# Kernel tuning notes

Hardware: AMD Instinct MI355X
Metric: run time of the kernel (lower is better)

The kernel has to match this reference:

```python
import jax, jax.numpy as jnp
import numpy as np

H, C = 4, 32            # heads, per-head channels (hidden_dim)
F_IN = 128
N_NODES = 50000
N_EDGES = 800000
N_GRAPHS = 64
EPS_SM = 1e-16          # PyG softmax denom eps
EPS_BN = 1e-5


def gat_layer(x, W, a_src, a_dst, b, src, dst, n):
    # x: [N, Fin]; W: [Fin, H*C]; a_src/a_dst: [H, C]; b: [H*C]
    h = (x @ W).reshape(n, H, C)                      # [N,H,C]
    e_src = jnp.einsum('nhc,hc->nh', h, a_src)        # [N,H]
    e_dst = jnp.einsum('nhc,hc->nh', h, a_dst)
    e = jax.nn.leaky_relu(e_src[src] + e_dst[dst], 0.2)  # [E,H]
    m = jax.lax.stop_gradient(jax.ops.segment_max(e, dst, num_segments=n))
    ex = jnp.exp(e - m[dst])
    denom = jax.ops.segment_sum(ex, dst, num_segments=n)
    alpha = ex / (denom[dst] + EPS_SM)                # softmax per destination node
    out = jax.ops.segment_sum(h[src] * alpha[..., None], dst, num_segments=n)
    return out.reshape(n, H * C) + b


def batchnorm(x, gamma, beta):
    # training-mode BN over the node dimension (biased variance)
    mu = x.mean(0)
    var = x.var(0)
    return (x - mu) * jax.lax.rsqrt(var + EPS_BN) * gamma + beta


def setup_inputs() -> dict:
    key = jax.random.key(0)
    ks = jax.random.split(key, 24)
    D = H * C  # 128

    def lin(k, fan_in, shape):
        return jax.random.normal(k, shape, jnp.float32) / np.sqrt(fan_in)

    inp = {
        'x': jax.random.normal(ks[0], (N_NODES, F_IN), jnp.float32),
        'edge_index': jax.random.randint(ks[1], (2, N_EDGES), 0, N_NODES, jnp.int64),
        'node_types': jax.random.randint(ks[2], (N_NODES,), 0, 2, jnp.int64),
        'batch': jnp.sort(jax.random.randint(ks[3], (N_NODES,), 0, N_GRAPHS, jnp.int64)),
        # GAT layer 1 (F_IN -> H*C)
        'W1': lin(ks[4], F_IN, (F_IN, D)), 'as1': lin(ks[5], C, (H, C)),
        'ad1': lin(ks[6], C, (H, C)), 'b1': jnp.zeros((D,), jnp.float32),
        'g1': jnp.ones((D,), jnp.float32), 'be1': jnp.zeros((D,), jnp.float32),
        # GAT layer 2 (D -> D)
        'W2': lin(ks[7], D, (D, D)), 'as2': lin(ks[8], C, (H, C)),
        'ad2': lin(ks[9], C, (H, C)), 'b2': jnp.zeros((D,), jnp.float32),
        'g2': jnp.ones((D,), jnp.float32), 'be2': jnp.zeros((D,), jnp.float32),
        # GAT layer 3 (D -> D)
        'W3': lin(ks[10], D, (D, D)), 'as3': lin(ks[11], C, (H, C)),
        'ad3': lin(ks[12], C, (H, C)), 'b3': jnp.zeros((D,), jnp.float32),
        'g3': jnp.ones((D,), jnp.float32), 'be3': jnp.zeros((D,), jnp.float32),
        # MLP head
        'fc1_w': lin(ks[13], D, (D, C)), 'fc1_b': jnp.zeros((C,), jnp.float32),
        'fc2_w': lin(ks[14], C, (C, 1)), 'fc2_b': jnp.zeros((1,), jnp.float32),
    }
    return inp


def reference(x, edge_index, node_types, batch,
              W1, as1, ad1, b1, g1, be1,
              W2, as2, ad2, b2, g2, be2,
              W3, as3, ad3, b3, g3, be3,
              fc1_w, fc1_b, fc2_w, fc2_b):
    n = x.shape[0]
    # PyG GATConv adds self-loops by default
    loops = jnp.arange(n, dtype=edge_index.dtype)
    src = jnp.concatenate([edge_index[0], loops])
    dst = jnp.concatenate([edge_index[1], loops])
    aw = jnp.where(node_types == 0, 1.5, 1.0).astype(x.dtype)[:, None]  # [N,1]

    h = gat_layer(x, W1, as1, ad1, b1, src, dst, n) * aw
    h = jax.nn.relu(batchnorm(h, g1, be1))
    h = gat_layer(h, W2, as2, ad2, b2, src, dst, n) * aw
    h = jax.nn.relu(batchnorm(h, g2, be2))
    h = gat_layer(h, W3, as3, ad3, b3, src, dst, n) * aw
    h = jax.nn.relu(batchnorm(h, g3, be3))

    # global mean pool over graphs
    sums = jax.ops.segment_sum(h, batch, num_segments=N_GRAPHS)
    cnt = jax.ops.segment_sum(jnp.ones((n,), h.dtype), batch, num_segments=N_GRAPHS)
    pooled = sums / jnp.maximum(cnt, 1.0)[:, None]     # [G, H*C]

    out = jax.nn.relu(pooled @ fc1_w + fc1_b) @ fc2_w + fc2_b  # [G, 1]
    return out
```

## Files before the change

kernel.cpp:

```cpp
#include <hip/hip_runtime.h>
#include <hip/hip_bf16.h>
#include <math.h>

#define NN 50000
#define EE 800000
#define ET_ 850000
#define NG 64
#define NB 196
#define PB 1024
#define GB 391
#define NBK 196
#define BCAP 5120
#define GATB 2048

typedef __attribute__((ext_vector_type(8))) short bf16x8;
typedef __attribute__((ext_vector_type(4))) float f32x4;
typedef __attribute__((ext_vector_type(4))) _Float16 h16x4;

__device__ __forceinline__ void bsplit(float v, ushort& h, ushort& l){
  unsigned u = __float_as_uint(v);
  unsigned hb = (u + 0x7fffu + ((u >> 16) & 1u)) >> 16;
  h = (ushort)hb;
  float hf = __uint_as_float(hb << 16);
  float r = v - hf;
  unsigned ur = __float_as_uint(r);
  l = (ushort)((ur + 0x7fffu + ((ur >> 16) & 1u)) >> 16);
}

__global__ __launch_bounds__(256) void convw(const float* __restrict__ W,
    ushort* __restrict__ wfrag){
  int idx = blockIdx.x*256 + threadIdx.x;
  if (idx >= 128*128) return;
  int c = idx & 127, k = idx >> 7;
  float v = W[idx];
  ushort h, lo;
  bsplit(v, h, lo);
  int dest = (((c>>4)*4 + (k>>5))*64 + (((k&31)>>3)<<4 | (c&15)))*8 + (k&7);
  wfrag[dest] = h;
  wfrag[16384 + dest] = lo;
}

__global__ __launch_bounds__(256) void convea(const float* __restrict__ W,
    const float* __restrict__ as_, const float* __restrict__ ad_,
    ushort* __restrict__ eafrag){
  const int t = threadIdx.x;
  const int kb = t >> 6, l = t & 63;
  const int col = l & 15, krow = (l >> 4) * 8;
  #pragma unroll
  for (int j = 0; j < 8; j++){
    int k = kb*32 + krow + j;
    float v = 0.f;
    if (col < 8){
      int h = col & 3;
      const float* a  = (col < 4) ? (as_ + h*32) : (ad_ + h*32);
      const float* wr = W + (size_t)k*128 + h*32;
      float acc = 0.f;
      #pragma unroll
      for (int c = 0; c < 32; c++) acc += wr[c]*a[c];
      v = acc;
    }
    ushort hi, lo;
    bsplit(v, hi, lo);
    eafrag[(kb*64 + l)*8 + j] = hi;
    eafrag[2048 + (kb*64 + l)*8 + j] = lo;
  }
}

__global__ __launch_bounds__(512) void gemm_fused(const float* __restrict__ X,
    const ushort* __restrict__ wfrag, const ushort* __restrict__ eafrag,
    const float* __restrict__ scale, const float* __restrict__ shift,
    _Float16* __restrict__ H, float* __restrict__ esrc, float* __restrict__ edst, int N){
  __shared__ ushort wl[32768];
  const int tid = threadIdx.x;
  #pragma unroll
  for (int i = 0; i < 8; i++){
    int e = (i*512 + tid) * 8;
    *(bf16x8*)(wl + e) = *(const bf16x8*)(wfrag + e);
  }
  const int w  = tid >> 6;
  const int l  = tid & 63;
  const int lr = l & 15;
  const int lg = l >> 4;
  const int lk = lg * 8;
  const int arow = blockIdx.x*128 + w*16 + lr;
  const bool avl = (arow < N);
  const size_t abase = (size_t)(avl ? arow : 0) * 128;
  bf16x8 ahi[4], alo[4];
  #pragma unroll
  for (int kb = 0; kb < 4; kb++){
    float a[8];
    if (avl){
      *(float4*)(a)   = *(const float4*)(X + abase + kb*32 + lk);
      *(float4*)(a+4) = *(const float4*)(X + abase + kb*32 + lk + 4);
    } else {
      #pragma unroll
      for (int j=0;j<8;j++) a[j] = 0.f;
    }
    if (scale){
      float s[8], b[8];
      *(float4*)(s)   = *(const float4*)(scale + kb*32 + lk);
      *(float4*)(s+4) = *(const float4*)(scale + kb*32 + lk + 4);
      *(float4*)(b)   = *(const float4*)(shift + kb*32 + lk);
      *(float4*)(b+4) = *(const float4*)(shift + kb*32 + lk + 4);
      #pragma unroll
      for (int j=0;j<8;j++) a[j] = fmaxf(fmaf(a[j], s[j], b[j]), 0.f);
    }
    #pragma unroll
    for (int j=0;j<8;j++){
      ushort hh2, ll2;
      bsplit(a[j], hh2, ll2);
      ahi[kb][j] = (short)hh2;
      alo[kb][j] = (short)ll2;
    }
  }
  __syncthreads();
  const int crowb = blockIdx.x*128 + w*16 + lg*4;
  #pragma unroll
  for (int ct = 0; ct < 8; ct++){
    f32x4 acc = {0.f,0.f,0.f,0.f};
    #pragma unroll
    for (int kb = 0; kb < 4; kb++){
      const int fi = ((ct*4 + kb)*64 + l) * 8;
      bf16x8 bhf = *(const bf16x8*)(wl + fi);
      bf16x8 blf = *(const bf16x8*)(wl + 16384 + fi);
      acc = __builtin_amdgcn_mfma_f32_16x16x32_bf16(ahi[kb], bhf, acc, 0, 0, 0);
      acc = __builtin_amdgcn_mfma_f32_16x16x32_bf16(ahi[kb], blf, acc, 0, 0, 0);
      acc = __builtin_amdgcn_mfma_f32_16x16x32_bf16(alo[kb], bhf, acc, 0, 0, 0);
    }
    #pragma unroll
    for (int j = 0; j < 4; j++){
      int r = crowb + j;
      if (r < N) H[(size_t)r*128 + ct*16 + lr] = (_Float16)acc[j];
    }
  }
  {
    f32x4 acc = {0.f,0.f,0.f,0.f};
    #pragma unroll
    for (int kb = 0; kb < 4; kb++){
      bf16x8 bhf = *(const bf16x8*)(eafrag + (kb*64 + l)*8);
      bf16x8 blf = *(const bf16x8*)(eafrag + 2048 + (kb*64 + l)*8);
      acc = __builtin_amdgcn_mfma_f32_16x16x32_bf16(ahi[kb], bhf, acc, 0, 0, 0);
      acc = __builtin_amdgcn_mfma_f32_16x16x32_bf16(ahi[kb], blf, acc, 0, 0, 0);
      acc = __builtin_amdgcn_mfma_f32_16x16x32_bf16(alo[kb], bhf, acc, 0, 0, 0);
    }
    if (lr < 8){
      #pragma unroll
      for (int j = 0; j < 4; j++){
        int r = crowb + j;
        if (r < N){
          if (lr < 4) esrc[r*4 + lr] = acc[j];
          else        edst[r*4 + lr - 4] = acc[j];
        }
      }
    }
  }
}

__global__ __launch_bounds__(256) void bin_scatter(const int* __restrict__ ei,
    int* __restrict__ btail, int2* __restrict__ bkt){
  __shared__ int cnt[NBK];
  __shared__ int base[NBK];
  const int t = threadIdx.x;
  for (int i = t; i < NBK; i += 256) cnt[i] = 0;
  __syncthreads();
  int sv[8], dv[8], bv[8], lr[8];
  const int e0 = blockIdx.x*2048;
  #pragma unroll
  for (int k = 0; k < 8; k++){
    int i = e0 + k*256 + t;
    sv[k] = -1;
    if (i < ET_){
      int s, d;
      if (i < EE){ s = ei[i]; d = ei[EE + i]; } else { s = i - EE; d = s; }
      sv[k] = s; dv[k] = d; bv[k] = d >> 8;
      lr[k] = atomicAdd(&cnt[bv[k]], 1);
    }
  }
  __syncthreads();
  for (int i = t; i < NBK; i += 256){
    int c = cnt[i];
    base[i] = c ? atomicAdd(&btail[i], c) : 0;
  }
  __syncthreads();
  #pragma unroll
  for (int k = 0; k < 8; k++){
    if (sv[k] >= 0){
      int p = base[bv[k]] + lr[k];
      if (p < BCAP) bkt[bv[k]*BCAP + p] = make_int2(sv[k], dv[k]);
    }
  }
}

__global__ __launch_bounds__(256) void bucket_count(const int* __restrict__ btail,
    const int2* __restrict__ bkt, int* __restrict__ cnt){
  __shared__ int c256[256];
  const int b = blockIdx.x, t = threadIdx.x;
  c256[t] = 0; __syncthreads();
  int n = btail[b]; if (n > BCAP) n = BCAP;
  for (int i = t; i < n; i += 256){
    int d = bkt[b*BCAP + i].y;
    atomicAdd(&c256[d & 255], 1);
  }
  __syncthreads();
  int node = b*256 + t;
  if (node < NN) cnt[node] = c256[t];
}

__global__ __launch_bounds__(256) void scan_partial(const int* __restrict__ cnt,
    int* __restrict__ rowptr, int* __restrict__ bsum){
  __shared__ int sh[256];
  const int t = threadIdx.x;
  const int i = blockIdx.x*256 + t;
  int v = (i < NN) ? cnt[i] : 0;
  sh[t] = v; __syncthreads();
  for (int o=1;o<256;o<<=1){
    int u = (t>=o) ? sh[t-o] : 0;
    __syncthreads();
    sh[t] += u;
    __syncthreads();
  }
  if (i < NN) rowptr[i] = sh[t] - v;
  if (t == 255) bsum[blockIdx.x] = sh[255];
}

__global__ __launch_bounds__(256) void scan_bsum(int* __restrict__ bsum){
  __shared__ int sh[256];
  const int t = threadIdx.x;
  int v = (t < NB) ? bsum[t] : 0;
  sh[t] = v; __syncthreads();
  for (int o=1;o<256;o<<=1){
    int u = (t>=o) ? sh[t-o] : 0;
    __syncthreads();
    sh[t] += u;
    __syncthreads();
  }
  if (t < NB) bsum[t] = sh[t] - v;
}

__global__ __launch_bounds__(256) void scan_add(int* __restrict__ rowptr,
    const int* __restrict__ bsum){
  const int i = blockIdx.x*256 + threadIdx.x;
  if (i < NN) rowptr[i] += bsum[blockIdx.x];
  if (i == NN) rowptr[NN] = ET_;
}

__global__ __launch_bounds__(256) void bucket_scatter(const int* __restrict__ btail,
    const int2* __restrict__ bkt, const int* __restrict__ rowptr,
    int* __restrict__ csr_src){
  __shared__ int h256[256];
  const int b = blockIdx.x, t = threadIdx.x;
  int node = b*256 + t;
  h256[t] = (node < NN) ? rowptr[node] : 0;
  __syncthreads();
  int n = btail[b]; if (n > BCAP) n = BCAP;
  for (int i = t; i < n; i += 256){
    int2 e = bkt[b*BCAP + i];
    int pos = atomicAdd(&h256[e.y & 255], 1);
    csr_src[pos] = e.x;
  }
}

__global__ __launch_bounds__(256) void gat_fused(const int* __restrict__ rowptr,
    const int* __restrict__ csr_src, const float* __restrict__ esrc,
    const float* __restrict__ edst, const _Float16* __restrict__ hbuf,
    const float* __restrict__ bias, const int* __restrict__ ntype,
    float* __restrict__ y, float* __restrict__ bnpart){
  __shared__ int2 pk[4][64][4];
  const int w    = threadIdx.x >> 6;
  const int lane = threadIdx.x & 63;
  const int c4   = (lane & 31) * 4;
  const int eh   = lane >> 5;
  const int head = (lane & 31) >> 3;
  const int2* pp = &pk[w][eh][head];

  float bs0=0.f,bs1=0.f,bs2=0.f,bs3=0.f,bq0=0.f,bq1=0.f,bq2=0.f,bq3=0.f;
  const float4 bb = *(const float4*)(bias + c4);

  for (int d = blockIdx.x*4 + w; d < NN; d += GATB*4){
    const int beg = rowptr[d], end = rowptr[d+1];
    const float4 ed4 = *(const float4*)(edst + (size_t)d*4);
    float dn0=0.f, dn1=0.f, dn2=0.f, dn3=0.f;
    float4 acc0 = make_float4(0.f,0.f,0.f,0.f);
    float4 acc1 = make_float4(0.f,0.f,0.f,0.f);

    for (int j0 = beg; j0 < end; j0 += 64){
      int j = j0 + lane;
      int s = d;
      float ex0=0.f, ex1=0.f, ex2=0.f, ex3=0.f;
      if (j < end){
        s = csr_src[j];
        float4 es = *(const float4*)(esrc + (size_t)s*4);
        float e0 = es.x + ed4.x; e0 = (e0 > 0.f) ? e0 : 0.2f*e0;
        float e1 = es.y + ed4.y; e1 = (e1 > 0.f) ? e1 : 0.2f*e1;
        float e2 = es.z + ed4.z; e2 = (e2 > 0.f) ? e2 : 0.2f*e2;
        float e3 = es.w + ed4.w; e3 = (e3 > 0.f) ? e3 : 0.2f*e3;
        ex0 = expf(e0); ex1 = expf(e1); ex2 = expf(e2); ex3 = expf(e3);
        dn0 += ex0; dn1 += ex1; dn2 += ex2; dn3 += ex3;
      }
      int4 w0 = make_int4(s, __float_as_int(ex0), s, __float_as_int(ex1));
      int4 w1 = make_int4(s, __float_as_int(ex2), s, __float_as_int(ex3));
      *(int4*)&pk[w][lane][0] = w0;
      *(int4*)&pk[w][lane][2] = w1;
      int cnt2 = end - j0; if (cnt2 > 64) cnt2 = 64;
      const int npair = (cnt2 + 1) >> 1;
      int p = 0;
      #pragma unroll 2
      for (; p + 2 <= npair; p += 2){
        int2 va = pp[p*8];
        int2 vb = pp[p*8 + 8];
        float wa = __int_as_float(va.y);
        float wb = __int_as_float(vb.y);
        h16x4 ha = *(const h16x4*)(hbuf + (size_t)va.x*128 + c4);
        h16x4 hb = *(const h16x4*)(hbuf + (size_t)vb.x*128 + c4);
        acc0.x = fmaf((float)ha.x, wa, acc0.x);
        acc0.y = fmaf((float)ha.y, wa, acc0.y);
        acc0.z = fmaf((float)ha.z, wa, acc0.z);
        acc0.w = fmaf((float)ha.w, wa, acc0.w);
        acc1.x = fmaf((float)hb.x, wb, acc1.x);
        acc1.y = fmaf((float)hb.y, wb, acc1.y);
        acc1.z = fmaf((float)hb.z, wb, acc1.z);
        acc1.w = fmaf((float)hb.w, wb, acc1.w);
      }
      if (p < npair){
        int2 va = pp[p*8];
        float wa = __int_as_float(va.y);
        h16x4 ha = *(const h16x4*)(hbuf + (size_t)va.x*128 + c4);
        acc0.x = fmaf((float)ha.x, wa, acc0.x);
        acc0.y = fmaf((float)ha.y, wa, acc0.y);
        acc0.z = fmaf((float)ha.z, wa, acc0.z);
        acc0.w = fmaf((float)ha.w, wa, acc0.w);
      }
    }
    #pragma unroll
    for (int o = 32; o; o >>= 1){
      dn0 += __shfl_xor(dn0, o);
      dn1 += __shfl_xor(dn1, o);
      dn2 += __shfl_xor(dn2, o);
      dn3 += __shfl_xor(dn3, o);
    }
    float dsel = (head==0) ? dn0 : (head==1) ? dn1 : (head==2) ? dn2 : dn3;
    float inv = 1.f / (dsel + 1e-16f);
    float4 acc;
    acc.x = acc0.x + acc1.x;
    acc.y = acc0.y + acc1.y;
    acc.z = acc0.z + acc1.z;
    acc.w = acc0.w + acc1.w;
    acc.x += __shfl_xor(acc.x, 32);
    acc.y += __shfl_xor(acc.y, 32);
    acc.z += __shfl_xor(acc.z, 32);
    acc.w += __shfl_xor(acc.w, 32);
    if (eh == 0){
      float aw = (ntype[d] == 0) ? 1.5f : 1.0f;
      float4 o4;
      o4.x = (acc.x*inv + bb.x) * aw;
      o4.y = (acc.y*inv + bb.y) * aw;
      o4.z = (acc.z*inv + bb.z) * aw;
      o4.w = (acc.w*inv + bb.w) * aw;
      *(float4*)(y + (size_t)d*128 + c4) = o4;
      bs0 += o4.x; bs1 += o4.y; bs2 += o4.z; bs3 += o4.w;
      bq0 += o4.x*o4.x; bq1 += o4.y*o4.y; bq2 += o4.z*o4.z; bq3 += o4.w*o4.w;
    }
  }
  __syncthreads();
  float* bnp = (float*)pk;
  if (eh == 0){
    float* q = bnp + (w*32 + (lane & 31))*8;
    q[0]=bs0; q[1]=bs1; q[2]=bs2; q[3]=bs3;
    q[4]=bq0; q[5]=bq1; q[6]=bq2; q[7]=bq3;
  }
  __syncthreads();
  const int t = threadIdx.x;
  const int c = t & 127, stat = t >> 7;
  float v = 0.f;
  #pragma unroll
  for (int ww = 0; ww < 4; ww++)
    v += bnp[(ww*32 + (c>>2))*8 + stat*4 + (c&3)];
  bnpart[(size_t)blockIdx.x*256 + t] = v;
}

__global__ __launch_bounds__(256) void bn_reduce(const float* __restrict__ bnpart,
    double* __restrict__ bnsum, double* __restrict__ bnsumsq){
  const int t = threadIdx.x, b = blockIdx.x;
  float acc = 0.f;
  #pragma unroll 4
  for (int j = 0; j < GATB/64; j++)
    acc += bnpart[(size_t)(b*(GATB/64) + j)*256 + t];
  const int c = t & 127;
  if (t < 128) atomicAdd(bnsum + c, (double)acc);
  else         atomicAdd(bnsumsq + c, (double)acc);
}

__global__ void bn_final(const double* __restrict__ bnsum, const double* __restrict__ bnsumsq,
    const float* __restrict__ gma, const float* __restrict__ bta,
    float* __restrict__ scale, float* __restrict__ shift, int N){
  int c = threadIdx.x;
  double mu  = bnsum[c] / N;
  double var = bnsumsq[c] / N - mu*mu;
  if (var < 0.0) var = 0.0;
  float inv = (float)(1.0 / sqrt(var + 1e-5));
  float sc  = inv * gma[c];
  scale[c] = sc;
  shift[c] = bta[c] - (float)mu * sc;
}

__global__ __launch_bounds__(256) void pool_partial(const float* __restrict__ y,
    const int* __restrict__ batch, const float* __restrict__ scale,
    const float* __restrict__ shift, float* __restrict__ pooled){
  const int t = threadIdx.x;
  const int c = t & 127;
  const int sub = t >> 7;
  const int per = (NN + PB - 1) / PB;
  const int n0 = blockIdx.x * per;
  int n1 = n0 + per; if (n1 > NN) n1 = NN;
  const float sc = scale[c], sh = shift[c];
  float acc = 0.f;
  int curg = -1;
  for (int n = n0 + sub; n < n1; n += 2){
    int g = batch[n];
    if (g != curg){
      if (curg >= 0) unsafeAtomicAdd(pooled + (size_t)curg*128 + c, acc);
      curg = g; acc = 0.f;
    }
    float v = y[(size_t)n*128 + c];
    acc += fmaxf(fmaf(v, sc, sh), 0.f);
  }
  if (curg >= 0) unsafeAtomicAdd(pooled + (size_t)curg*128 + c, acc);
}

__global__ __launch_bounds__(128) void mlp_head(const float* __restrict__ pooled,
    const int* __restrict__ batch, const float* __restrict__ fc1w,
    const float* __restrict__ fc1b, const float* __restrict__ fc2w,
    const float* __restrict__ fc2b, float* __restrict__ out){
  __shared__ float psh[128];
  __shared__ float hid[32];
  const int g = blockIdx.x, t = threadIdx.x;
  int lo = 0, hi = NN;
  while (lo < hi){ int mid = (lo+hi)>>1; if (batch[mid] < g) lo = mid+1; else hi = mid; }
  const int beg = lo;
  lo = beg; hi = NN;
  while (lo < hi){ int mid = (lo+hi)>>1; if (batch[mid] < g+1) lo = mid+1; else hi = mid; }
  int cntn = lo - beg; if (cntn < 1) cntn = 1;
  psh[t] = pooled[(size_t)g*128 + t] / (float)cntn;
  __syncthreads();
  if (t < 32){
    float a = fc1b[t];
    for (int k=0;k<128;k++) a += psh[k]*fc1w[k*32+t];
    a = (a > 0.f) ? a : 0.f;
    hid[t] = a * fc2w[t];
  }
  __syncthreads();
  if (t == 0){
    float sacc = fc2b[0];
    #pragma unroll
    for (int j=0;j<32;j++) sacc += hid[j];
    out[g] = sacc;
  }
}

extern "C" void kernel_launch(void* const* d_in, const int* in_sizes, int n_in,
                              void* d_out, int out_size, void* d_ws, size_t ws_size,
                              hipStream_t stream){
  const float* x     = (const float*)d_in[0];
  const int*   ei    = (const int*)d_in[1];
  const int*   ntype = (const int*)d_in[2];
  const int*   batch = (const int*)d_in[3];
  const float* Wl[3]  = {(const float*)d_in[4],  (const float*)d_in[10], (const float*)d_in[16]};
  const float* asl[3] = {(const float*)d_in[5],  (const float*)d_in[11], (const float*)d_in[17]};
  const float* adl[3] = {(const float*)d_in[6],  (const float*)d_in[12], (const float*)d_in[18]};
  const float* bl[3]  = {(const float*)d_in[7],  (const float*)d_in[13], (const float*)d_in[19]};
  const float* gl[3]  = {(const float*)d_in[8],  (const float*)d_in[14], (const float*)d_in[20]};
  const float* bel[3] = {(const float*)d_in[9],  (const float*)d_in[15], (const float*)d_in[21]};
  const float* fc1w = (const float*)d_in[22];
  const float* fc1b = (const float*)d_in[23];
  const float* fc2w = (const float*)d_in[24];
  const float* fc2b = (const float*)d_in[25];

  char* base = (char*)d_ws;
  size_t off = 0;
  auto alloc = [&](size_t bytes)->char*{
    size_t o = (off + 255) & ~(size_t)255; off = o + bytes; return base + o;
  };
  _Float16* hbuf = (_Float16*)alloc((size_t)NN*128*2);
  float* y       = (float*)alloc((size_t)NN*128*4);
  ushort* wfrag  = (ushort*)alloc((size_t)32768*2);
  ushort* eafrag = (ushort*)alloc((size_t)4096*2);
  float* esrc    = (float*)alloc((size_t)NN*4*4);
  float* edst    = (float*)alloc((size_t)NN*4*4);
  int*   cnt     = (int*)  alloc((size_t)NN*4);
  int*   rowptr  = (int*)  alloc((size_t)(NN+1)*4);
  int*   csr_src = (int*)  alloc((size_t)ET_*4);
  int*   btail   = (int*)  alloc((size_t)NBK*4);
  int2*  bkt     = (int2*) alloc((size_t)NBK*BCAP*8);
  int*   bsum    = (int*)  alloc((size_t)NB*4);
  float* bnpart  = (float*)alloc((size_t)GATB*256*4);
  double* bnsum  = (double*)alloc(128*8);
  double* bnsumsq= (double*)alloc(128*8);
  float* scale   = (float*)alloc(128*4);
  float* shift   = (float*)alloc(128*4);
  float* pooled  = (float*)alloc((size_t)NG*128*4);
  if (off > ws_size) return;

  hipMemsetAsync(btail, 0, (size_t)NBK*4, stream);
  hipMemsetAsync(pooled, 0, (size_t)NG*128*4, stream);
  bin_scatter<<<(ET_+2047)/2048, 256, 0, stream>>>(ei, btail, bkt);
  bucket_count<<<NBK, 256, 0, stream>>>(btail, bkt, cnt);
  scan_partial<<<NB, 256, 0, stream>>>(cnt, rowptr, bsum);
  scan_bsum<<<1, 256, 0, stream>>>(bsum);
  scan_add<<<NB, 256, 0, stream>>>(rowptr, bsum);
  bucket_scatter<<<NBK, 256, 0, stream>>>(btail, bkt, rowptr, csr_src);

  for (int l = 0; l < 3; l++){
    const float* in = (l==0) ? x : y;
    const float* scl = (l==0) ? nullptr : scale;
    const float* shf = (l==0) ? nullptr : shift;
    hipMemsetAsync(bnsum, 0, 128*8*2, stream);
    convw<<<64, 256, 0, stream>>>(Wl[l], wfrag);
    convea<<<1, 256, 0, stream>>>(Wl[l], asl[l], adl[l], eafrag);
    gemm_fused<<<GB, 512, 0, stream>>>(in, wfrag, eafrag, scl, shf,
                                       hbuf, esrc, edst, NN);
    gat_fused<<<GATB, 256, 0, stream>>>(rowptr, csr_src, esrc, edst, hbuf,
                                        bl[l], ntype, y, bnpart);
    bn_reduce<<<64, 256, 0, stream>>>(bnpart, bnsum, bnsumsq);
    bn_final<<<1, 128, 0, stream>>>(bnsum, bnsumsq, gl[l], bel[l], scale, shift, NN);
  }
  pool_partial<<<PB, 256, 0, stream>>>(y, batch, scale, shift, pooled);
  mlp_head<<<NG, 128, 0, stream>>>(pooled, batch, fc1w, fc1b, fc2w, fc2b, (float*)d_out);
}
```

Measured before the change: 435.2 us.

## Widen GAT gather to 8 channels per lane, 4 edges per wave; merge weight-prep kernels

The aggregation kernel now has each lane gather 8 fp16 channels (16-byte loads), so a wave processes 4 edges at once instead of 2. Partial sums are reduced across lanes with two xor-shuffle steps. The BN partial-sum layout is adjusted to match the new lane mapping. The grid grows from 2048 to 6144 blocks, and the two small weight-conversion kernels are merged into one launch to save a kernel launch per layer. With 6144 blocks, bn_reduce's 64 blocks now read 96 partials each.

Result: no change. 432.3 us (-0.7%).

```diff
diff --git a/kernel.cpp b/kernel.cpp
--- a/kernel.cpp
+++ b/kernel.cpp
@@ -11,11 +11,11 @@
 #define GB 391
 #define NBK 196
 #define BCAP 5120
-#define GATB 2048
+#define GATB 6144
 
 typedef __attribute__((ext_vector_type(8))) short bf16x8;
 typedef __attribute__((ext_vector_type(4))) float f32x4;
-typedef __attribute__((ext_vector_type(4))) _Float16 h16x4;
+typedef __attribute__((ext_vector_type(8))) _Float16 h16x8;
 
 __device__ __forceinline__ void bsplit(float v, ushort& h, ushort& l){
   unsigned u = __float_as_uint(v);
@@ -27,42 +27,40 @@
   l = (ushort)((ur + 0x7fffu + ((ur >> 16) & 1u)) >> 16);
 }
 
-__global__ __launch_bounds__(256) void convw(const float* __restrict__ W,
-    ushort* __restrict__ wfrag){
-  int idx = blockIdx.x*256 + threadIdx.x;
-  if (idx >= 128*128) return;
-  int c = idx & 127, k = idx >> 7;
-  float v = W[idx];
-  ushort h, lo;
-  bsplit(v, h, lo);
-  int dest = (((c>>4)*4 + (k>>5))*64 + (((k&31)>>3)<<4 | (c&15)))*8 + (k&7);
-  wfrag[dest] = h;
-  wfrag[16384 + dest] = lo;
-}
-
-__global__ __launch_bounds__(256) void convea(const float* __restrict__ W,
+__global__ __launch_bounds__(256) void convwa(const float* __restrict__ W,
     const float* __restrict__ as_, const float* __restrict__ ad_,
-    ushort* __restrict__ eafrag){
+    ushort* __restrict__ wfrag, ushort* __restrict__ eafrag){
   const int t = threadIdx.x;
-  const int kb = t >> 6, l = t & 63;
-  const int col = l & 15, krow = (l >> 4) * 8;
-  #pragma unroll
-  for (int j = 0; j < 8; j++){
-    int k = kb*32 + krow + j;
-    float v = 0.f;
-    if (col < 8){
-      int h = col & 3;
-      const float* a  = (col < 4) ? (as_ + h*32) : (ad_ + h*32);
-      const float* wr = W + (size_t)k*128 + h*32;
-      float acc = 0.f;
-      #pragma unroll
-      for (int c = 0; c < 32; c++) acc += wr[c]*a[c];
-      v = acc;
-    }
-    ushort hi, lo;
-    bsplit(v, hi, lo);
-    eafrag[(kb*64 + l)*8 + j] = hi;
-    eafrag[2048 + (kb*64 + l)*8 + j] = lo;
+  if (blockIdx.x < 64){
+    int idx = blockIdx.x*256 + t;
+    int c = idx & 127, k = idx >> 7;
+    float v = W[idx];
+    ushort h, lo;
+    bsplit(v, h, lo);
+    int dest = (((c>>4)*4 + (k>>5))*64 + (((k&31)>>3)<<4 | (c&15)))*8 + (k&7);
+    wfrag[dest] = h;
+    wfrag[16384 + dest] = lo;
+  } else {
+    const int kb = t >> 6, l = t & 63;
+    const int col = l & 15, krow = (l >> 4) * 8;
+    #pragma unroll
+    for (int j = 0; j < 8; j++){
+      int k = kb*32 + krow + j;
+      float v = 0.f;
+      if (col < 8){
+        int h = col & 3;
+        const float* a  = (col < 4) ? (as_ + h*32) : (ad_ + h*32);
+        const float* wr = W + (size_t)k*128 + h*32;
+        float acc = 0.f;
+        #pragma unroll
+        for (int c = 0; c < 32; c++) acc += wr[c]*a[c];
+        v = acc;
+      }
+      ushort hi, lo;
+      bsplit(v, hi, lo);
+      eafrag[(kb*64 + l)*8 + j] = hi;
+      eafrag[2048 + (kb*64 + l)*8 + j] = lo;
+    }
   }
 }
 
@@ -268,20 +266,24 @@
   __shared__ int2 pk[4][64][4];
   const int w    = threadIdx.x >> 6;
   const int lane = threadIdx.x & 63;
-  const int c4   = (lane & 31) * 4;
-  const int eh   = lane >> 5;
-  const int head = (lane & 31) >> 3;
-  const int2* pp = &pk[w][eh][head];
-
-  float bs0=0.f,bs1=0.f,bs2=0.f,bs3=0.f,bq0=0.f,bq1=0.f,bq2=0.f,bq3=0.f;
-  const float4 bb = *(const float4*)(bias + c4);
+  const int e    = lane >> 4;
+  const int c8   = lane & 15;
+  const int hd   = c8 >> 2;
+  const int2* pg = &pk[w][e][hd];
+
+  float bs[8], bq[8];
+  #pragma unroll
+  for (int k=0;k<8;k++){ bs[k]=0.f; bq[k]=0.f; }
+  const float4 bbA = *(const float4*)(bias + c8*8);
+  const float4 bbB = *(const float4*)(bias + c8*8 + 4);
 
   for (int d = blockIdx.x*4 + w; d < NN; d += GATB*4){
     const int beg = rowptr[d], end = rowptr[d+1];
     const float4 ed4 = *(const float4*)(edst + (size_t)d*4);
     float dn0=0.f, dn1=0.f, dn2=0.f, dn3=0.f;
-    float4 acc0 = make_float4(0.f,0.f,0.f,0.f);
-    float4 acc1 = make_float4(0.f,0.f,0.f,0.f);
+    float acc[8];
+    #pragma unroll
+    for (int k=0;k<8;k++) acc[k]=0.f;
 
     for (int j0 = beg; j0 < end; j0 += 64){
       int j = j0 + lane;
@@ -302,33 +304,14 @@
       *(int4*)&pk[w][lane][0] = w0;
       *(int4*)&pk[w][lane][2] = w1;
       int cnt2 = end - j0; if (cnt2 > 64) cnt2 = 64;
-      const int npair = (cnt2 + 1) >> 1;
-      int p = 0;
+      const int ngrp = (cnt2 + 3) >> 2;
       #pragma unroll 2
-      for (; p + 2 <= npair; p += 2){
-        int2 va = pp[p*8];
-        int2 vb = pp[p*8 + 8];
-        float wa = __int_as_float(va.y);
-        float wb = __int_as_float(vb.y);
-        h16x4 ha = *(const h16x4*)(hbuf + (size_t)va.x*128 + c4);
-        h16x4 hb = *(const h16x4*)(hbuf + (size_t)vb.x*128 + c4);
-        acc0.x = fmaf((float)ha.x, wa, acc0.x);
-        acc0.y = fmaf((float)ha.y, wa, acc0.y);
-        acc0.z = fmaf((float)ha.z, wa, acc0.z);
-        acc0.w = fmaf((float)ha.w, wa, acc0.w);
-        acc1.x = fmaf((float)hb.x, wb, acc1.x);
-        acc1.y = fmaf((float)hb.y, wb, acc1.y);
-        acc1.z = fmaf((float)hb.z, wb, acc1.z);
-        acc1.w = fmaf((float)hb.w, wb, acc1.w);
-      }
-      if (p < npair){
-        int2 va = pp[p*8];
-        float wa = __int_as_float(va.y);
-        h16x4 ha = *(const h16x4*)(hbuf + (size_t)va.x*128 + c4);
-        acc0.x = fmaf((float)ha.x, wa, acc0.x);
-        acc0.y = fmaf((float)ha.y, wa, acc0.y);
-        acc0.z = fmaf((float)ha.z, wa, acc0.z);
-        acc0.w = fmaf((float)ha.w, wa, acc0.w);
+      for (int g = 0; g < ngrp; g++){
+        int2 v = pg[g*16];
+        float wg = __int_as_float(v.y);
+        h16x8 hv = *(const h16x8*)(hbuf + (size_t)v.x*128 + c8*8);
+        #pragma unroll
+        for (int k=0;k<8;k++) acc[k] = fmaf((float)hv[k], wg, acc[k]);
       }
     }
     #pragma unroll
@@ -338,35 +321,36 @@
       dn2 += __shfl_xor(dn2, o);
       dn3 += __shfl_xor(dn3, o);
     }
-    float dsel = (head==0) ? dn0 : (head==1) ? dn1 : (head==2) ? dn2 : dn3;
+    float dsel = (hd==0) ? dn0 : (hd==1) ? dn1 : (hd==2) ? dn2 : dn3;
     float inv = 1.f / (dsel + 1e-16f);
-    float4 acc;
-    acc.x = acc0.x + acc1.x;
-    acc.y = acc0.y + acc1.y;
-    acc.z = acc0.z + acc1.z;
-    acc.w = acc0.w + acc1.w;
-    acc.x += __shfl_xor(acc.x, 32);
-    acc.y += __shfl_xor(acc.y, 32);
-    acc.z += __shfl_xor(acc.z, 32);
-    acc.w += __shfl_xor(acc.w, 32);
-    if (eh == 0){
+    #pragma unroll
+    for (int k=0;k<8;k++){
+      acc[k] += __shfl_xor(acc[k], 16);
+      acc[k] += __shfl_xor(acc[k], 32);
+    }
+    if (e == 0){
       float aw = (ntype[d] == 0) ? 1.5f : 1.0f;
-      float4 o4;
-      o4.x = (acc.x*inv + bb.x) * aw;
-      o4.y = (acc.y*inv + bb.y) * aw;
-      o4.z = (acc.z*inv + bb.z) * aw;
-      o4.w = (acc.w*inv + bb.w) * aw;
-      *(float4*)(y + (size_t)d*128 + c4) = o4;
-      bs0 += o4.x; bs1 += o4.y; bs2 += o4.z; bs3 += o4.w;
-      bq0 += o4.x*o4.x; bq1 += o4.y*o4.y; bq2 += o4.z*o4.z; bq3 += o4.w*o4.w;
+      float o8[8];
+      o8[0] = (acc[0]*inv + bbA.x) * aw;
+      o8[1] = (acc[1]*inv + bbA.y) * aw;
+      o8[2] = (acc[2]*inv + bbA.z) * aw;
+      o8[3] = (acc[3]*inv + bbA.w) * aw;
+      o8[4] = (acc[4]*inv + bbB.x) * aw;
+      o8[5] = (acc[5]*inv + bbB.y) * aw;
+      o8[6] = (acc[6]*inv + bbB.z) * aw;
+      o8[7] = (acc[7]*inv + bbB.w) * aw;
+      *(float4*)(y + (size_t)d*128 + c8*8)     = make_float4(o8[0],o8[1],o8[2],o8[3]);
+      *(float4*)(y + (size_t)d*128 + c8*8 + 4) = make_float4(o8[4],o8[5],o8[6],o8[7]);
+      #pragma unroll
+      for (int k=0;k<8;k++){ bs[k] += o8[k]; bq[k] += o8[k]*o8[k]; }
     }
   }
   __syncthreads();
   float* bnp = (float*)pk;
-  if (eh == 0){
-    float* q = bnp + (w*32 + (lane & 31))*8;
-    q[0]=bs0; q[1]=bs1; q[2]=bs2; q[3]=bs3;
-    q[4]=bq0; q[5]=bq1; q[6]=bq2; q[7]=bq3;
+  if (e == 0){
+    float* q = bnp + (w*16 + c8)*16;
+    #pragma unroll
+    for (int k=0;k<8;k++){ q[k] = bs[k]; q[8+k] = bq[k]; }
   }
   __syncthreads();
   const int t = threadIdx.x;
@@ -374,7 +358,7 @@
   float v = 0.f;
   #pragma unroll
   for (int ww = 0; ww < 4; ww++)
-    v += bnp[(ww*32 + (c>>2))*8 + stat*4 + (c&3)];
+    v += bnp[(ww*16 + (c>>3))*16 + stat*8 + (c&7)];
   bnpart[(size_t)blockIdx.x*256 + t] = v;
 }
 
@@ -514,8 +498,7 @@
     const float* scl = (l==0) ? nullptr : scale;
     const float* shf = (l==0) ? nullptr : shift;
     hipMemsetAsync(bnsum, 0, 128*8*2, stream);
-    convw<<<64, 256, 0, stream>>>(Wl[l], wfrag);
-    convea<<<1, 256, 0, stream>>>(Wl[l], asl[l], adl[l], eafrag);
+    convwa<<<65, 256, 0, stream>>>(Wl[l], asl[l], adl[l], wfrag, eafrag);
     gemm_fused<<<GB, 512, 0, stream>>>(in, wfrag, eafrag, scl, shf,
                                        hbuf, esrc, edst, NN);
     gat_fused<<<GATB, 256, 0, stream>>>(rowptr, csr_src, esrc, edst, hbuf,
```
